# Performance work log

Measured on AMD Instinct MI355X. Metric: run time of the kernel, lower is better.

The kernel has to match this reference:

```python
import jax, jax.numpy as jnp
import numpy as np

B, I, C, H, W = 8, 16, 256, 64, 64  # batch, instances, channels(=in=out), spatial


def setup_inputs() -> dict:
    key = jax.random.key(0)
    ks = jax.random.split(key, 8)
    x = jax.random.normal(ks[0], (B, C, H, W), dtype=jnp.float32)
    masks = jax.random.uniform(ks[1], (B, I, H, W), dtype=jnp.float32)
    # conv_feat: 1x1 conv C->C  -> weight [C_out, C_in]
    Wf = jax.random.normal(ks[2], (C, C), dtype=jnp.float32) * 0.02
    bf = jax.random.normal(ks[3], (C,), dtype=jnp.float32) * 0.02
    # conv_mask: grouped 1x1 conv, groups=I, each 1 -> C channels -> weight [I, C]
    Wm = jax.random.normal(ks[4], (I, C), dtype=jnp.float32) * 0.02
    bm = jax.random.normal(ks[5], (I, C), dtype=jnp.float32) * 0.02
    # conv_out: 1x1 conv C->C
    Wo = jax.random.normal(ks[6], (C, C), dtype=jnp.float32) * 0.02
    bo = jax.random.normal(ks[7], (C,), dtype=jnp.float32) * 0.02
    gamma = jnp.float32(0.5)  # torch init is 0.0; use nonzero so baseline is nontrivial
    return {"x": x, "masks": masks, "Wf": Wf, "bf": bf, "Wm": Wm, "bm": bm,
            "Wo": Wo, "bo": bo, "gamma": gamma}


def reference(x, masks, Wf, bf, Wm, bm, Wo, bo, gamma):
    b, i, h, w = masks.shape
    c = Wf.shape[0]
    # conv_feat: 1x1 conv == per-pixel matmul
    feat = jnp.einsum('bchw,oc->bohw', x, Wf) + bf[:, None, None]  # [B,C,H,W]
    # grouped 1x1 conv_mask: instance i channel -> C channels
    mc = (masks[:, :, None, :, :] * Wm[None, :, :, None, None]
          + bm[None, :, :, None, None])                              # [B,I,C,H,W]
    # softmax over (C*H*W) per instance, as in masks.view(B, I, -1)
    mc = jax.nn.softmax(mc.reshape(b, i, -1), axis=-1).reshape(b, i, c, h, w)
    # loop sum_i conv_out(feat * mask_i)  ==  conv_out_W @ (feat * sum_i mask_i) + I*bias
    msum = mc.sum(axis=1)                                            # [B,C,H,W]
    out = jnp.einsum('bchw,oc->bohw', feat * msum, Wo) + (i * bo)[:, None, None]
    return gamma * out + x
```

## Files before the change

### kernel.cpp

```cpp
#include <hip/hip_runtime.h>


#define NB 8
#define NI 16
#define NC 256
#define HWSZ 4096
#define PT 32

typedef __attribute__((ext_vector_type(8))) short short8;
typedef __attribute__((ext_vector_type(4))) short short4v;
typedef __attribute__((ext_vector_type(4))) float f32x4;

static __device__ inline short f2bf(float f) {
    unsigned u = __builtin_bit_cast(unsigned, f);
    u += 0x7fffu + ((u >> 16) & 1u);
    return (short)(u >> 16);
}
static __device__ inline float bf2f(short h) {
    unsigned u = ((unsigned)(unsigned short)h) << 16;
    return __builtin_bit_cast(float, u);
}

__global__ __launch_bounds__(256)
void setup_kernel(const float* __restrict__ masks, const float* __restrict__ Wm,
                  const float* __restrict__ bm, const float* __restrict__ Wf,
                  const float* __restrict__ Wo, short* __restrict__ Ahat,
                  short* __restrict__ WfB, short* __restrict__ WoB) {
    const int blk = blockIdx.x, t = threadIdx.x;
    if (blk >= NB * NI) {
        const int wb = blk - NB * NI;
#pragma unroll
        for (int r = 0; r < 2; ++r) {
            int fid = (wb * 256 + t) * 2 + r;
            const float* src = (fid < 16384) ? Wf : Wo;
            short* dst       = (fid < 16384) ? WfB : WoB;
            int e = (fid & 16383) * 4;
            float4 v = *(const float4*)(src + e);
            short4v o = { f2bf(v.x), f2bf(v.y), f2bf(v.z), f2bf(v.w) };
            *(short4v*)(dst + e) = o;
        }
        return;
    }
    const int bi = blk;
    const int b  = bi >> 4;
    const int i  = bi & (NI - 1);
    const float* m = masks + (size_t)bi * HWSZ;

    float s1 = 0.f, s2 = 0.f, s3 = 0.f, s4 = 0.f, s5 = 0.f, s6 = 0.f;
    for (int e = t; e < HWSZ; e += 256) {
        float v = m[e];
        float v2 = v * v, v3 = v2 * v;
        s1 += v; s2 += v2; s3 += v3;
        s4 += v2 * v2; s5 += v2 * v3; s6 += v3 * v3;
    }
    __shared__ float red[7][4];
    float sv[6] = { s1, s2, s3, s4, s5, s6 };
#pragma unroll
    for (int k = 0; k < 6; ++k) {
        float v = sv[k];
#pragma unroll
        for (int off = 32; off > 0; off >>= 1) v += __shfl_down(v, off, 64);
        if ((t & 63) == 0) red[k][t >> 6] = v;
    }
    __syncthreads();
    const float S1 = red[0][0] + red[0][1] + red[0][2] + red[0][3];
    const float S2 = red[1][0] + red[1][1] + red[1][2] + red[1][3];
    const float S3 = red[2][0] + red[2][1] + red[2][2] + red[2][3];
    const float S4 = red[3][0] + red[3][1] + red[3][2] + red[3][3];
    const float S5 = red[4][0] + red[4][1] + red[4][2] + red[4][3];
    const float S6 = red[5][0] + red[5][1] + red[5][2] + red[5][3];

    const int c = t;
    const float w  = Wm[i * NC + c];
    const float eb = __expf(bm[i * NC + c]);
    const float poly = (float)HWSZ
        + w * (S1 + w * (0.5f * S2 + w * ((1.f / 6.f) * S3
        + w * ((1.f / 24.f) * S4 + w * ((1.f / 120.f) * S5
        + w * ((1.f / 720.f) * S6))))));
    float v = eb * poly;
#pragma unroll
    for (int off = 32; off > 0; off >>= 1) v += __shfl_down(v, off, 64);
    if ((t & 63) == 0) red[6][t >> 6] = v;
    __syncthreads();
    const float Z = red[6][0] + red[6][1] + red[6][2] + red[6][3];
    const float a = eb / Z;
    short4v av = { f2bf(a), f2bf(a * w), f2bf(a * w * w * 0.5f),
                   f2bf(a * w * w * w * (1.f / 6.f)) };
    *(short4v*)(Ahat + ((size_t)(b * NC + c)) * 64 + i * 4) = av;
}

__global__ __launch_bounds__(256, 4)
void main_kernel(const float* __restrict__ x, const float* __restrict__ masks,
                 const float* __restrict__ bf_, const float* __restrict__ bo,
                 const float* __restrict__ gamma_p,
                 const short* __restrict__ WfB, const short* __restrict__ WoB,
                 const short* __restrict__ Ahat, float* __restrict__ out) {
    const int blk  = blockIdx.x;
    const int b    = blk >> 7;
    const int hw0  = (blk & 127) << 5;
    const int t    = threadIdx.x;
    const int lane = t & 63;
    const int ln15 = lane & 15;
    const int q    = lane >> 4;
    const int wo0  = (t >> 6) << 6;

    __shared__ __align__(16) short smem[19200];
    short* sA = smem;
    short* sM = smem + 8448;
    short* sZ = smem + 10752;

    const float* xbase = x + ((size_t)b * NC) * HWSZ + hw0;

    const int cth = t >> 3;
    const int qf  = t & 7;
    float4 xr[8];
#pragma unroll
    for (int it = 0; it < 8; ++it)
        xr[it] = *(const float4*)(xbase + (size_t)(it * 32 + cth) * HWSZ + qf * 4);

    const short* Ab = Ahat + ((size_t)b * NC) * 64;
    short8 a0f[2][4];
#pragma unroll
    for (int ks = 0; ks < 2; ++ks)
#pragma unroll
        for (int ot = 0; ot < 4; ++ot)
            a0f[ks][ot] = *(const short8*)(Ab + (wo0 + ot * 16 + ln15) * 64
                                           + ks * 32 + q * 8);

    {
        const int i  = t >> 4;
        const int p2 = (t & 15) * 2;
        const float* mp = masks + ((size_t)(b * NI + i)) * HWSZ + hw0 + p2;
        float m0 = mp[0], m1 = mp[1];
        float m0s = m0 * m0, m1s = m1 * m1;
        short4v v0 = { (short)0x3F80, f2bf(m0), f2bf(m0s), f2bf(m0s * m0) };
        short4v v1 = { (short)0x3F80, f2bf(m1), f2bf(m1s), f2bf(m1s * m1) };
        *(short4v*)(sM + p2 * 72 + i * 4) = v0;
        *(short4v*)(sM + (p2 + 1) * 72 + i * 4) = v1;
    }

#pragma unroll
    for (int it = 0; it < 8; ++it) {
        const int c = it * 32 + cth;
        sA[(qf * 4 + 0) * 264 + c] = f2bf(xr[it].x);
        sA[(qf * 4 + 1) * 264 + c] = f2bf(xr[it].y);
        sA[(qf * 4 + 2) * 264 + c] = f2bf(xr[it].z);
        sA[(qf * 4 + 3) * 264 + c] = f2bf(xr[it].w);
    }
    __syncthreads();

    f32x4 macc[4][2];
#pragma unroll
    for (int ot = 0; ot < 4; ++ot)
#pragma unroll
        for (int pt = 0; pt < 2; ++pt) macc[ot][pt] = (f32x4)0.f;
#pragma unroll
    for (int ks = 0; ks < 2; ++ks) {
        short8 bfr[2];
#pragma unroll
        for (int pt = 0; pt < 2; ++pt)
            bfr[pt] = *(const short8*)(sM + (pt * 16 + ln15) * 72 + ks * 32 + q * 8);
#pragma unroll
        for (int ot = 0; ot < 4; ++ot)
#pragma unroll
            for (int pt = 0; pt < 2; ++pt)
                macc[ot][pt] = __builtin_amdgcn_mfma_f32_16x16x32_bf16(
                    a0f[ks][ot], bfr[pt], macc[ot][pt], 0, 0, 0);
    }

    f32x4 feat[4][2];
#pragma unroll
    for (int ot = 0; ot < 4; ++ot)
#pragma unroll
        for (int pt = 0; pt < 2; ++pt) feat[ot][pt] = (f32x4)0.f;
#pragma unroll 4
    for (int ks = 0; ks < 8; ++ks) {
        short8 af[4], bfr[2];
#pragma unroll
        for (int ot = 0; ot < 4; ++ot)
            af[ot] = *(const short8*)(WfB + (wo0 + ot * 16 + ln15) * NC + ks * 32 + q * 8);
#pragma unroll
        for (int pt = 0; pt < 2; ++pt)
            bfr[pt] = *(const short8*)(sA + (pt * 16 + ln15) * 264 + ks * 32 + q * 8);
#pragma unroll
        for (int ot = 0; ot < 4; ++ot)
#pragma unroll
            for (int pt = 0; pt < 2; ++pt)
                feat[ot][pt] = __builtin_amdgcn_mfma_f32_16x16x32_bf16(
                    af[ot], bfr[pt], feat[ot][pt], 0, 0, 0);
    }

#pragma unroll
    for (int ot = 0; ot < 4; ++ot) {
        float4 bv = *(const float4*)(bf_ + wo0 + ot * 16 + q * 4);
        float b4[4] = { bv.x, bv.y, bv.z, bv.w };
#pragma unroll
        for (int pt = 0; pt < 2; ++pt) {
            short4v zz;
#pragma unroll
            for (int r = 0; r < 4; ++r)
                zz[r] = f2bf((feat[ot][pt][r] + b4[r]) * macc[ot][pt][r]);
            *(short4v*)(sZ + (pt * 16 + ln15) * 264 + wo0 + ot * 16 + q * 4) = zz;
        }
    }
    __syncthreads();

    f32x4 oacc[4][2];
#pragma unroll
    for (int ot = 0; ot < 4; ++ot)
#pragma unroll
        for (int pt = 0; pt < 2; ++pt) oacc[ot][pt] = (f32x4)0.f;
#pragma unroll 4
    for (int ks = 0; ks < 8; ++ks) {
        short8 af[4], bfr[2];
#pragma unroll
        for (int ot = 0; ot < 4; ++ot)
            af[ot] = *(const short8*)(WoB + (wo0 + ot * 16 + ln15) * NC + ks * 32 + q * 8);
#pragma unroll
        for (int pt = 0; pt < 2; ++pt)
            bfr[pt] = *(const short8*)(sZ + (pt * 16 + ln15) * 264 + ks * 32 + q * 8);
#pragma unroll
        for (int ot = 0; ot < 4; ++ot)
#pragma unroll
            for (int pt = 0; pt < 2; ++pt)
                oacc[ot][pt] = __builtin_amdgcn_mfma_f32_16x16x32_bf16(
                    af[ot], bfr[pt], oacc[ot][pt], 0, 0, 0);
    }

#pragma unroll
    for (int ot = 0; ot < 4; ++ot)
#pragma unroll
        for (int pt = 0; pt < 2; ++pt)
#pragma unroll
            for (int r = 0; r < 4; ++r)
                smem[(wo0 + ot * 16 + q * 4 + r) * 36 + pt * 16 + ln15] =
                    f2bf(oacc[ot][pt][r]);
    __syncthreads();

    float4 xv[8];
#pragma unroll
    for (int it = 0; it < 8; ++it) {
        int idx = it * 256 + t;
        xv[it] = *(const float4*)(xbase + (size_t)(idx >> 3) * HWSZ + (idx & 7) * 4);
    }
    const float g = gamma_p[0];
    float* ob = out + ((size_t)b * NC) * HWSZ + hw0;
#pragma unroll
    for (int it = 0; it < 8; ++it) {
        int idx = it * 256 + t;
        int o = idx >> 3, pq = idx & 7;
        short4v zb = *(const short4v*)(smem + o * 36 + pq * 4);
        float bov = 16.0f * bo[o];
        float4 r;
        r.x = g * (bf2f(zb[0]) + bov) + xv[it].x;
        r.y = g * (bf2f(zb[1]) + bov) + xv[it].y;
        r.z = g * (bf2f(zb[2]) + bov) + xv[it].z;
        r.w = g * (bf2f(zb[3]) + bov) + xv[it].w;
        *(float4*)(ob + (size_t)o * HWSZ + pq * 4) = r;
    }
}

extern "C" void kernel_launch(void* const* d_in, const int* in_sizes, int n_in,
                              void* d_out, int out_size, void* d_ws, size_t ws_size,
                              hipStream_t stream) {
    const float* x     = (const float*)d_in[0];
    const float* masks = (const float*)d_in[1];
    const float* Wf    = (const float*)d_in[2];
    const float* bf    = (const float*)d_in[3];
    const float* Wm    = (const float*)d_in[4];
    const float* bm    = (const float*)d_in[5];
    const float* Wo    = (const float*)d_in[6];
    const float* bo    = (const float*)d_in[7];
    const float* gamma = (const float*)d_in[8];
    float* out = (float*)d_out;

    short* ws   = (short*)d_ws;
    short* WfB  = ws;
    short* WoB  = WfB + NC * NC;
    short* Ahat = WoB + NC * NC;

    hipLaunchKernelGGL(setup_kernel, dim3(NB * NI + 64), dim3(256), 0, stream,
                       masks, Wm, bm, Wf, Wo, Ahat, WfB, WoB);
    hipLaunchKernelGGL(main_kernel, dim3(NB * (HWSZ / PT)), dim3(256), 0, stream,
                       x, masks, bf, bo, gamma, WfB, WoB, Ahat, out);
}
```

Baseline: 138.7 us.

## Pre-swizzle weights into MFMA fragment order and reuse x registers for residual

The setup kernel now writes Wf, Wo and the mask-coefficient matrix in MFMA fragment order, so each lane's short8 load in the main kernel is contiguous and coalesced. The mask MFMA moves to after the feat GEMM and runs per output tile, which cuts live registers. The z tile reuses the sA shared buffer, shrinking LDS from about 38KB to 21KB, which may raise occupancy. The residual x values stay in registers from the initial load instead of being re-read from global memory, at the cost of more live registers and an extra barrier.

```diff
diff --git a/kernel.cpp b/kernel.cpp
--- a/kernel.cpp
+++ b/kernel.cpp
@@ -21,24 +21,29 @@
     return __builtin_bit_cast(float, u);
 }
 
+
 __global__ __launch_bounds__(256)
 void setup_kernel(const float* __restrict__ masks, const float* __restrict__ Wm,
                   const float* __restrict__ bm, const float* __restrict__ Wf,
-                  const float* __restrict__ Wo, short* __restrict__ Ahat,
-                  short* __restrict__ WfB, short* __restrict__ WoB) {
+                  const float* __restrict__ Wo, short* __restrict__ AhatF,
+                  short* __restrict__ WfF, short* __restrict__ WoF) {
     const int blk = blockIdx.x, t = threadIdx.x;
     if (blk >= NB * NI) {
-        const int wb = blk - NB * NI;
-#pragma unroll
-        for (int r = 0; r < 2; ++r) {
-            int fid = (wb * 256 + t) * 2 + r;
-            const float* src = (fid < 16384) ? Wf : Wo;
-            short* dst       = (fid < 16384) ? WfB : WoB;
-            int e = (fid & 16383) * 4;
-            float4 v = *(const float4*)(src + e);
-            short4v o = { f2bf(v.x), f2bf(v.y), f2bf(v.z), f2bf(v.w) };
-            *(short4v*)(dst + e) = o;
-        }
+        const int pid = (blk - NB * NI) * 256 + t;
+        const float* src = (pid < 8192) ? Wf : Wo;
+        short* dst       = (pid < 8192) ? WfF : WoF;
+        const int r  = pid & 8191;
+        const int l  = r & 63;
+        const int ot = (r >> 6) & 3;
+        const int ks = (r >> 8) & 7;
+        const int w  = (r >> 11) & 3;
+        const int o  = w * 64 + ot * 16 + (l & 15);
+        const int c0 = ks * 32 + (l >> 4) * 8;
+        float4 v0 = *(const float4*)(src + o * NC + c0);
+        float4 v1 = *(const float4*)(src + o * NC + c0 + 4);
+        short8 p = { f2bf(v0.x), f2bf(v0.y), f2bf(v0.z), f2bf(v0.w),
+                     f2bf(v1.x), f2bf(v1.y), f2bf(v1.z), f2bf(v1.w) };
+        *(short8*)(dst + r * 8) = p;
         return;
     }
     const int bi = blk;
@@ -84,17 +89,24 @@
     __syncthreads();
     const float Z = red[6][0] + red[6][1] + red[6][2] + red[6][3];
     const float a = eb / Z;
+    const int wv   = c >> 6;
+    const int ot   = (c >> 4) & 3;
+    const int ln15 = c & 15;
+    const int ks   = i >> 3;
+    const int qq   = (i >> 1) & 3;
+    const int l    = qq * 16 + ln15;
+    const int js   = (i & 1) * 4;
     short4v av = { f2bf(a), f2bf(a * w), f2bf(a * w * w * 0.5f),
                    f2bf(a * w * w * w * (1.f / 6.f)) };
-    *(short4v*)(Ahat + ((size_t)(b * NC + c)) * 64 + i * 4) = av;
+    *(short4v*)(AhatF + ((((b * 4 + wv) * 2 + ks) * 4 + ot) * 64 + l) * 8 + js) = av;
 }
 
 __global__ __launch_bounds__(256, 4)
 void main_kernel(const float* __restrict__ x, const float* __restrict__ masks,
                  const float* __restrict__ bf_, const float* __restrict__ bo,
                  const float* __restrict__ gamma_p,
-                 const short* __restrict__ WfB, const short* __restrict__ WoB,
-                 const short* __restrict__ Ahat, float* __restrict__ out) {
+                 const short* __restrict__ WfF, const short* __restrict__ WoF,
+                 const short* __restrict__ AhatF, float* __restrict__ out) {
     const int blk  = blockIdx.x;
     const int b    = blk >> 7;
     const int hw0  = (blk & 127) << 5;
@@ -102,12 +114,12 @@
     const int lane = t & 63;
     const int ln15 = lane & 15;
     const int q    = lane >> 4;
-    const int wo0  = (t >> 6) << 6;
-
-    __shared__ __align__(16) short smem[19200];
+    const int w    = t >> 6;
+    const int wo0  = w << 6;
+
+    __shared__ __align__(16) short smem[10752];
     short* sA = smem;
     short* sM = smem + 8448;
-    short* sZ = smem + 10752;
 
     const float* xbase = x + ((size_t)b * NC) * HWSZ + hw0;
 
@@ -117,15 +129,6 @@
 #pragma unroll
     for (int it = 0; it < 8; ++it)
         xr[it] = *(const float4*)(xbase + (size_t)(it * 32 + cth) * HWSZ + qf * 4);
-
-    const short* Ab = Ahat + ((size_t)b * NC) * 64;
-    short8 a0f[2][4];
-#pragma unroll
-    for (int ks = 0; ks < 2; ++ks)
-#pragma unroll
-        for (int ot = 0; ot < 4; ++ot)
-            a0f[ks][ot] = *(const short8*)(Ab + (wo0 + ot * 16 + ln15) * 64
-                                           + ks * 32 + q * 8);
 
     {
         const int i  = t >> 4;
@@ -149,25 +152,6 @@
     }
     __syncthreads();
 
-    f32x4 macc[4][2];
-#pragma unroll
-    for (int ot = 0; ot < 4; ++ot)
-#pragma unroll
-        for (int pt = 0; pt < 2; ++pt) macc[ot][pt] = (f32x4)0.f;
-#pragma unroll
-    for (int ks = 0; ks < 2; ++ks) {
-        short8 bfr[2];
-#pragma unroll
-        for (int pt = 0; pt < 2; ++pt)
-            bfr[pt] = *(const short8*)(sM + (pt * 16 + ln15) * 72 + ks * 32 + q * 8);
-#pragma unroll
-        for (int ot = 0; ot < 4; ++ot)
-#pragma unroll
-            for (int pt = 0; pt < 2; ++pt)
-                macc[ot][pt] = __builtin_amdgcn_mfma_f32_16x16x32_bf16(
-                    a0f[ks][ot], bfr[pt], macc[ot][pt], 0, 0, 0);
-    }
-
     f32x4 feat[4][2];
 #pragma unroll
     for (int ot = 0; ot < 4; ++ot)
@@ -178,7 +162,7 @@
         short8 af[4], bfr[2];
 #pragma unroll
         for (int ot = 0; ot < 4; ++ot)
-            af[ot] = *(const short8*)(WfB + (wo0 + ot * 16 + ln15) * NC + ks * 32 + q * 8);
+            af[ot] = *(const short8*)(WfF + (((w * 8 + ks) * 4 + ot) * 64 + lane) * 8);
 #pragma unroll
         for (int pt = 0; pt < 2; ++pt)
             bfr[pt] = *(const short8*)(sA + (pt * 16 + ln15) * 264 + ks * 32 + q * 8);
@@ -189,18 +173,40 @@
                 feat[ot][pt] = __builtin_amdgcn_mfma_f32_16x16x32_bf16(
                     af[ot], bfr[pt], feat[ot][pt], 0, 0, 0);
     }
-
-#pragma unroll
-    for (int ot = 0; ot < 4; ++ot) {
-        float4 bv = *(const float4*)(bf_ + wo0 + ot * 16 + q * 4);
-        float b4[4] = { bv.x, bv.y, bv.z, bv.w };
-#pragma unroll
-        for (int pt = 0; pt < 2; ++pt) {
-            short4v zz;
-#pragma unroll
-            for (int r = 0; r < 4; ++r)
-                zz[r] = f2bf((feat[ot][pt][r] + b4[r]) * macc[ot][pt][r]);
-            *(short4v*)(sZ + (pt * 16 + ln15) * 264 + wo0 + ot * 16 + q * 4) = zz;
+    __syncthreads();
+
+    {
+        short8 mfr[2][2];
+#pragma unroll
+        for (int ks = 0; ks < 2; ++ks)
+#pragma unroll
+            for (int pt = 0; pt < 2; ++pt)
+                mfr[ks][pt] = *(const short8*)(sM + (pt * 16 + ln15) * 72
+                                               + ks * 32 + q * 8);
+        const short* Ab = AhatF + (size_t)b * 2048 * 8;
+#pragma unroll
+        for (int ot = 0; ot < 4; ++ot) {
+            f32x4 macc[2];
+            macc[0] = (f32x4)0.f; macc[1] = (f32x4)0.f;
+#pragma unroll
+            for (int ks = 0; ks < 2; ++ks) {
+                short8 a0 = *(const short8*)(Ab + (((w * 2 + ks) * 4 + ot) * 64
+                                                   + lane) * 8);
+#pragma unroll
+                for (int pt = 0; pt < 2; ++pt)
+                    macc[pt] = __builtin_amdgcn_mfma_f32_16x16x32_bf16(
+                        a0, mfr[ks][pt], macc[pt], 0, 0, 0);
+            }
+            float4 bv = *(const float4*)(bf_ + wo0 + ot * 16 + q * 4);
+            float b4[4] = { bv.x, bv.y, bv.z, bv.w };
+#pragma unroll
+            for (int pt = 0; pt < 2; ++pt) {
+                short4v zz;
+#pragma unroll
+                for (int r = 0; r < 4; ++r)
+                    zz[r] = f2bf((feat[ot][pt][r] + b4[r]) * macc[pt][r]);
+                *(short4v*)(sA + (pt * 16 + ln15) * 264 + wo0 + ot * 16 + q * 4) = zz;
+            }
         }
     }
     __syncthreads();
@@ -215,10 +221,10 @@
         short8 af[4], bfr[2];
 #pragma unroll
         for (int ot = 0; ot < 4; ++ot)
-            af[ot] = *(const short8*)(WoB + (wo0 + ot * 16 + ln15) * NC + ks * 32 + q * 8);
+            af[ot] = *(const short8*)(WoF + (((w * 8 + ks) * 4 + ot) * 64 + lane) * 8);
 #pragma unroll
         for (int pt = 0; pt < 2; ++pt)
-            bfr[pt] = *(const short8*)(sZ + (pt * 16 + ln15) * 264 + ks * 32 + q * 8);
+            bfr[pt] = *(const short8*)(sA + (pt * 16 + ln15) * 264 + ks * 32 + q * 8);
 #pragma unroll
         for (int ot = 0; ot < 4; ++ot)
 #pragma unroll
@@ -226,6 +232,7 @@
                 oacc[ot][pt] = __builtin_amdgcn_mfma_f32_16x16x32_bf16(
                     af[ot], bfr[pt], oacc[ot][pt], 0, 0, 0);
     }
+    __syncthreads();
 
 #pragma unroll
     for (int ot = 0; ot < 4; ++ot)
@@ -237,26 +244,19 @@
                     f2bf(oacc[ot][pt][r]);
     __syncthreads();
 
-    float4 xv[8];
-#pragma unroll
-    for (int it = 0; it < 8; ++it) {
-        int idx = it * 256 + t;
-        xv[it] = *(const float4*)(xbase + (size_t)(idx >> 3) * HWSZ + (idx & 7) * 4);
-    }
     const float g = gamma_p[0];
     float* ob = out + ((size_t)b * NC) * HWSZ + hw0;
 #pragma unroll
     for (int it = 0; it < 8; ++it) {
-        int idx = it * 256 + t;
-        int o = idx >> 3, pq = idx & 7;
-        short4v zb = *(const short4v*)(smem + o * 36 + pq * 4);
+        const int o = it * 32 + cth;
+        short4v zb = *(const short4v*)(smem + o * 36 + qf * 4);
         float bov = 16.0f * bo[o];
         float4 r;
-        r.x = g * (bf2f(zb[0]) + bov) + xv[it].x;
-        r.y = g * (bf2f(zb[1]) + bov) + xv[it].y;
-        r.z = g * (bf2f(zb[2]) + bov) + xv[it].z;
-        r.w = g * (bf2f(zb[3]) + bov) + xv[it].w;
-        *(float4*)(ob + (size_t)o * HWSZ + pq * 4) = r;
+        r.x = g * (bf2f(zb[0]) + bov) + xr[it].x;
+        r.y = g * (bf2f(zb[1]) + bov) + xr[it].y;
+        r.z = g * (bf2f(zb[2]) + bov) + xr[it].z;
+        r.w = g * (bf2f(zb[3]) + bov) + xr[it].w;
+        *(float4*)(ob + (size_t)o * HWSZ + qf * 4) = r;
     }
 }
 
@@ -274,13 +274,13 @@
     const float* gamma = (const float*)d_in[8];
     float* out = (float*)d_out;
 
-    short* ws   = (short*)d_ws;
-    short* WfB  = ws;
-    short* WoB  = WfB + NC * NC;
-    short* Ahat = WoB + NC * NC;
+    short* ws    = (short*)d_ws;
+    short* WfF   = ws;
+    short* WoF   = WfF + 65536;
+    short* AhatF = WoF + 65536;
 
     hipLaunchKernelGGL(setup_kernel, dim3(NB * NI + 64), dim3(256), 0, stream,
-                       masks, Wm, bm, Wf, Wo, Ahat, WfB, WoB);
+                       masks, Wm, bm, Wf, Wo, AhatF, WfF, WoF);
     hipLaunchKernelGGL(main_kernel, dim3(NB * (HWSZ / PT)), dim3(256), 0, stream,
-                       x, masks, bf, bo, gamma, WfB, WoB, Ahat, out);
-}
+                       x, masks, bf, bo, gamma, WfF, WoF, AhatF, out);
+}
```

After: 118.0 us. 1.18x faster.
